# Kernel optimization log

Measured on AMD Instinct MI355X. Metric: run time of the kernel, lower is better.

Reference implementation:

```python
import jax, jax.numpy as jnp
import numpy as np

B, N, K = 4, 2048, 32
U, TU = 512, 128
RADII = (0.1, 0.3, 0.5)
FILTERS = [512, 256, 170]  # U // (i+1) for depth=3
BN_RS = 1.0 / np.sqrt(1.0 + 1e-3)  # inference BN with mean=0, var=1, keras eps=1e-3


def setup_inputs() -> dict:
    key = jax.random.key(0)
    ks = jax.random.split(key, 16)
    rn = lambda k, shape, s: jax.random.normal(k, shape, jnp.float32) * s
    d = {
        "pts": jax.random.normal(ks[0], (B, N, 3), jnp.float32),
        # T-Net params
        "t_cw": rn(ks[1], (3, TU), 0.3), "t_cb": jnp.zeros((TU,), jnp.float32),
        "t_g1": jnp.ones((TU,), jnp.float32), "t_b1": jnp.zeros((TU,), jnp.float32),
        "t_d1w": rn(ks[2], (TU, TU), 0.1), "t_d1b": jnp.zeros((TU,), jnp.float32),
        "t_g2": jnp.ones((TU,), jnp.float32), "t_b2": jnp.zeros((TU,), jnp.float32),
        "t_d2w": rn(ks[3], (TU, 9), 0.3), "t_d2b": jnp.zeros((9,), jnp.float32),
        # PCE conv1 + residual conv
        "c1_w": rn(ks[4], (9, U), 0.2), "c1_b": jnp.zeros((U,), jnp.float32),
        "c1_g": jnp.ones((U,), jnp.float32), "c1_beta": jnp.zeros((U,), jnp.float32),
        "res_w": rn(ks[5], (U, U), 0.05), "res_b": jnp.zeros((U,), jnp.float32),
    }
    fin = U
    for i, f in enumerate(FILTERS):
        d[f"blk{i}_w"] = rn(ks[6 + i], (fin, f), 0.05)
        d[f"blk{i}_b"] = jnp.zeros((f,), jnp.float32)
        d[f"blk{i}_g"] = jnp.ones((f,), jnp.float32)
        d[f"blk{i}_beta"] = jnp.zeros((f,), jnp.float32)
        fin = f
    return d


def _bn(x, g, b):
    # inference BN with moving_mean=0, moving_var=1: (x-0)/sqrt(1+eps)*g + b
    return x * (BN_RS * g) + b


def reference(pts, t_cw, t_cb, t_g1, t_b1, t_d1w, t_d1b, t_g2, t_b2, t_d2w, t_d2b,
              c1_w, c1_b, c1_g, c1_beta, res_w, res_b,
              blk0_w, blk0_b, blk0_g, blk0_beta,
              blk1_w, blk1_b, blk1_g, blk1_beta,
              blk2_w, blk2_b, blk2_g, blk2_beta):
    silu = jax.nn.silu  # keras 'swish'
    # ---- OrthogonalTNet (dropout = identity at inference) ----
    x = silu(_bn(jnp.einsum('bnd,de->bne', pts, t_cw) + t_cb, t_g1, t_b1))  # [B,N,TU]
    x = x.max(axis=1)                                                        # GlobalMaxPool1D
    x = silu(_bn(x @ t_d1w + t_d1b, t_g2, t_b2))
    T = (x @ t_d2w + t_d2b).reshape(-1, 3, 3)
    pc = jnp.einsum('bnd,bde->bne', pts, T)                                  # [B,N,3]
    # ---- pairwise distances [B,N,N] ----
    sq = jnp.sum(pc * pc, axis=-1)
    d2 = sq[:, :, None] + sq[:, None, :] - 2.0 * jnp.einsum('bnd,bmd->bnm', pc, pc)
    dist = jnp.sqrt(jnp.maximum(d2, 0.0))
    # ---- multi-scale grouping: radius mask -> top_k -> gather ----
    groups = []
    for r in RADII:
        mask = (dist <= r).astype(jnp.float32)
        idx = jax.lax.top_k(mask, K)[1]                                      # [B,N,K]
        groups.append(jax.vmap(lambda p, i: p[i])(pc, idx))                  # [B,N,K,3]
    f = jnp.concatenate(groups, axis=-1)                                     # [B,N,K,9]
    # ---- 1x1 conv stack (Dense over channel dim), dropout = identity ----
    f = silu(_bn(f @ c1_w + c1_b, c1_g, c1_beta))                            # [B,N,K,U]
    f = f + (f @ res_w + res_b)                                              # residual
    for w, b, g, beta in ((blk0_w, blk0_b, blk0_g, blk0_beta),
                          (blk1_w, blk1_b, blk1_g, blk1_beta),
                          (blk2_w, blk2_b, blk2_g, blk2_beta)):
        f = silu(_bn(f @ w + b, g, beta))
    Bv, Nv, Kv, Cv = f.shape
    f = f.reshape(Bv, Nv, Kv * Cv)                                           # [B,N,K*170]
    return f.max(axis=1)                                                     # GlobalMaxPool1D -> [B,5440]
```

## Files before the change

kernel.cpp:

```cpp
#include <hip/hip_runtime.h>
#include <math.h>

#define BN_RS 0.9995003746877732f

typedef unsigned short u16;
typedef _Float16 f16;
typedef __attribute__((ext_vector_type(8))) _Float16 h8v;
typedef __attribute__((ext_vector_type(4))) _Float16 h4v;
typedef __attribute__((ext_vector_type(2))) __fp16 fp16x2;
typedef __attribute__((ext_vector_type(4))) float f32x4;

__device__ __forceinline__ unsigned f2mono(float f){
  unsigned u = __float_as_uint(f);
  return (u & 0x80000000u) ? ~u : (u | 0x80000000u);
}
__device__ __forceinline__ float mono2f(unsigned m){
  unsigned u = (m & 0x80000000u) ? (m & 0x7FFFFFFFu) : ~m;
  return __uint_as_float(u);
}
__device__ __forceinline__ float silu_fast(float x){
  float e = __expf(-x);
  return x * __builtin_amdgcn_rcpf(1.f + e);
}
__device__ __forceinline__ float silu_f64(float x){
  double e = exp(-(double)x);
  return (float)((double)x / (1.0 + e));
}
__device__ __forceinline__ h4v pkrtz4(float a, float b, float c, float d){
  fp16x2 lo = __builtin_amdgcn_cvt_pkrtz(a, b);
  fp16x2 hi = __builtin_amdgcn_cvt_pkrtz(c, d);
  unsigned lu = __builtin_bit_cast(unsigned, lo);
  unsigned hu = __builtin_bit_cast(unsigned, hi);
  unsigned long long packed = ((unsigned long long)hu << 32) | lu;
  return __builtin_bit_cast(h4v, packed);
}

constexpr size_t OFF_T9   = 0;
constexpr size_t OFF_XM   = 1024;
constexpr size_t OFF_PC4  = 4096;
constexpr size_t OFF_OUT  = 139264;
constexpr size_t OFF_C1T  = 227328;
constexpr size_t OFF_B0C  = 262144;
constexpr size_t OFF_B1T  = 1310720;
constexpr size_t OFF_B2T  = 1572864;
constexpr size_t OFF_BS1  = 1662976;
constexpr size_t OFF_BS0  = 1667072;
constexpr size_t OFF_BSB1 = 1669120;
constexpr size_t OFF_BSB2 = 1670144;
constexpr size_t OFF_F9   = 1703936;

__global__ void tnet1_kernel(const float* __restrict__ pts, const float* __restrict__ t_cw,
                             const float* __restrict__ t_cb, const float* __restrict__ t_g1,
                             const float* __restrict__ t_b1, unsigned* __restrict__ xm_mono){
  int u = threadIdx.x;
  int b = blockIdx.x;
  int slice = blockIdx.y * blockDim.y + threadIdx.y;
  float w0 = t_cw[u], w1 = t_cw[128+u], w2 = t_cw[256+u];
  float cb = t_cb[u];
  float sc = __fmul_rn(BN_RS, t_g1[u]);
  float b1 = t_b1[u];
  float mx = -INFINITY;
  const float* P = pts + ((size_t)b*2048 + (size_t)slice*128)*3;
  for (int n = 0; n < 128; ++n){
    float y = __fadd_rn(__fadd_rn(__fmul_rn(P[n*3+0], w0), __fmul_rn(P[n*3+1], w1)),
                        __fmul_rn(P[n*3+2], w2));
    y = __fadd_rn(y, cb);
    y = __fadd_rn(__fmul_rn(y, sc), b1);
    mx = fmaxf(mx, silu_f64(y));
  }
  atomicMax(&xm_mono[b*128+u], f2mono(mx));
}

__global__ void tnet2_kernel(const unsigned* __restrict__ xm_mono,
                             const float* __restrict__ d1w, const float* __restrict__ d1b,
                             const float* __restrict__ g2, const float* __restrict__ b2,
                             const float* __restrict__ d2w, const float* __restrict__ d2b,
                             float* __restrict__ T9){
  __shared__ float xs[128], x2s[128];
  int u = threadIdx.x, b = blockIdx.x;
  xs[u] = mono2f(xm_mono[b*128+u]);
  __syncthreads();
  double acc = (double)d1b[u];
  for (int v = 0; v < 128; ++v) acc += (double)xs[v] * (double)d1w[v*128+u];
  double sc = (double)__fmul_rn(BN_RS, g2[u]);
  acc = acc*sc + (double)b2[u];
  double e = exp(-acc);
  x2s[u] = (float)(acc / (1.0 + e));
  __syncthreads();
  if (u < 9){
    double t = (double)d2b[u];
    for (int v = 0; v < 128; ++v) t += (double)x2s[v] * (double)d2w[v*9+u];
    T9[b*9+u] = (float)t;
  }
}

__global__ void pc_kernel(const float* __restrict__ pts, const float* __restrict__ T9,
                          float4* __restrict__ pc4){
  int i = blockIdx.x*blockDim.x + threadIdx.x;
  int b = i >> 11;
  const float* p = pts + (size_t)i*3;
  float x = p[0], y = p[1], z = p[2];
  const float* T = T9 + b*9;
  float px = __fadd_rn(__fadd_rn(__fmul_rn(x, T[0]), __fmul_rn(y, T[3])), __fmul_rn(z, T[6]));
  float py = __fadd_rn(__fadd_rn(__fmul_rn(x, T[1]), __fmul_rn(y, T[4])), __fmul_rn(z, T[7]));
  float pz = __fadd_rn(__fadd_rn(__fmul_rn(x, T[2]), __fmul_rn(y, T[5])), __fmul_rn(z, T[8]));
  float sq = __fadd_rn(__fadd_rn(__fmul_rn(px, px), __fmul_rn(py, py)), __fmul_rn(pz, pz));
  pc4[i] = make_float4(px, py, pz, sq);
}

__global__ __launch_bounds__(256) void group_kernel(const float4* __restrict__ pc4,
                                                    f16* __restrict__ f9){
  __shared__ float4 pcl[2048];
  __shared__ int ones[4][3][32];
  __shared__ int zer [4][3][32];
  const float RAD[3] = {0.1f, 0.3f, 0.5f};
  int tid = threadIdx.x, wave = tid >> 6, lane = tid & 63;
  int bid = blockIdx.x;
  int b = bid >> 9, n0 = (bid & 511) * 4;
  const float4* src = pc4 + (size_t)b*2048;
  for (int x = tid; x < 2048; x += 256) pcl[x] = src[x];
  __syncthreads();

  int n = n0 + wave;
  float4 pi = pcl[n];
  float xi = pi.x, yi = pi.y, zi = pi.z, sqi = pi.w;
  int c1[3] = {0,0,0}, c0[3] = {0,0,0};
  unsigned long long lt = (1ULL << lane) - 1ULL;

  for (int ch = 0; ch < 32; ++ch){
    int j = ch*64 + lane;
    float4 pj = pcl[j];
    float dot = __fadd_rn(__fadd_rn(__fmul_rn(xi, pj.x), __fmul_rn(yi, pj.y)),
                          __fmul_rn(zi, pj.z));
    float d2 = __fsub_rn(__fadd_rn(sqi, pj.w), __fmul_rn(2.f, dot));
    float dist = sqrtf(fmaxf(d2, 0.f));
    #pragma unroll
    for (int ri = 0; ri < 3; ++ri){
      bool in = (dist <= RAD[ri]);
      unsigned long long m = __ballot(in);
      int pc_lt = (int)__popcll(m & lt);
      if (c1[ri] < 32){
        int pos = c1[ri] + pc_lt;
        if (in && pos < 32) ones[wave][ri][pos] = j;
      }
      if (c0[ri] < 32){
        int pos = c0[ri] + (int)(lane - pc_lt);
        if (!in && pos < 32) zer[wave][ri][pos] = j;
      }
      int t1 = (int)__popcll(m);
      c1[ri] += t1;
      c0[ri] += 64 - t1;
    }
    if (c1[0] >= 32 && c1[1] >= 32 && c1[2] >= 32 &&
        c0[0] >= 32 && c0[1] >= 32 && c0[2] >= 32) break;
  }
  __syncthreads();

  if (lane < 32){
    h8v va, vb;
    #pragma unroll
    for (int t = 0; t < 8; ++t){ va[t] = (f16)0.f; vb[t] = (f16)0.f; }
    #pragma unroll
    for (int ri = 0; ri < 3; ++ri){
      int cc = c1[ri] < 32 ? c1[ri] : 32;
      int sel = (lane < cc) ? ones[wave][ri][lane] : zer[wave][ri][lane - cc];
      float4 p = pcl[sel];
      if (ri == 0){ va[0]=(f16)p.x; va[1]=(f16)p.y; va[2]=(f16)p.z; }
      if (ri == 1){ va[3]=(f16)p.x; va[4]=(f16)p.y; va[5]=(f16)p.z; }
      if (ri == 2){ va[6]=(f16)p.x; va[7]=(f16)p.y; vb[0]=(f16)p.z; }
    }
    f16* dst = f9 + (((size_t)(b*2048 + n) * 32 + lane) << 4);
    *(h8v*)dst = va;
    *(h8v*)(dst + 8) = vb;
  }
}

__device__ __forceinline__ void pack_frag(const float* __restrict__ src, f16* __restrict__ dst,
                                          int CO, int CI, int COr, int CIr,
                                          const float* __restrict__ g,
                                          int i0, int stride){
  int NT = CI >> 5;
  int total = (CO >> 4) * NT * 512;
  for (int x = i0; x < total; x += stride){
    int j = x & 7, lane = (x >> 3) & 63;
    int t = (x >> 9) % NT, sct = x / (NT << 9);
    int co = sct*16 + (lane & 15);
    int ci = t*32 + (lane >> 4)*8 + j;
    float v = 0.f;
    if (co < COr && ci < CIr){
      v = src[ci*COr + co];
      if (g) v *= BN_RS * g[co];
    }
    dst[x] = (f16)v;
  }
}

__global__ void prep_kernel(const float* __restrict__ c1w,
                            const float* __restrict__ b0w, const float* __restrict__ b1w,
                            const float* __restrict__ b2w,
                            const float* __restrict__ c1_b, const float* __restrict__ c1_g, const float* __restrict__ c1_be,
                            const float* __restrict__ res_b,
                            const float* __restrict__ b0_b, const float* __restrict__ b0_g, const float* __restrict__ b0_be,
                            const float* __restrict__ b1_b, const float* __restrict__ b1_g, const float* __restrict__ b1_be,
                            const float* __restrict__ b2_b, const float* __restrict__ b2_g, const float* __restrict__ b2_be,
                            f16* __restrict__ c1F, f16* __restrict__ b1F, f16* __restrict__ b2F,
                            float* __restrict__ bs1, float* __restrict__ bs0,
                            float* __restrict__ bsb1, float* __restrict__ bsb2){
  int i0 = blockIdx.x*blockDim.x + threadIdx.x;
  int stride = gridDim.x*blockDim.x;
  pack_frag(c1w,  c1F,  512,  32, 512,   9, c1_g, i0, stride);
  pack_frag(b1w,  b1F,  256, 512, 256, 512, b1_g, i0, stride);
  pack_frag(b2w,  b2F,  176, 256, 170, 256, b2_g, i0, stride);
  for (int x = i0; x < 512; x += stride){
    bs1[x] = c1_b[x]*(BN_RS*c1_g[x]) + c1_be[x];
    float s = b0_b[x];
    for (int m = 0; m < 512; ++m) s = fmaf(res_b[m], b0w[m*512 + x], s);
    bs0[x] = s*(BN_RS*b0_g[x]) + b0_be[x];
  }
  for (int x = i0; x < 256; x += stride) bsb1[x] = b1_b[x]*(BN_RS*b1_g[x]) + b1_be[x];
  for (int x = i0; x < 176; x += stride)
    bsb2[x] = (x < 170) ? b2_b[x]*(BN_RS*b2_g[x]) + b2_be[x] : 0.f;
}

__global__ __launch_bounds__(256) void composeb0_kernel(const float* __restrict__ resw,
                                                        const float* __restrict__ b0w,
                                                        const float* __restrict__ b0_g,
                                                        f16* __restrict__ b0C){
  int x = blockIdx.x*blockDim.x + threadIdx.x;
  int j = x & 7, lane = (x >> 3) & 63;
  int t = (x >> 9) & 15, sct = x >> 13;
  int co = sct*16 + (lane & 15);
  int ci = t*32 + (lane >> 4)*8 + j;
  float s = b0w[ci*512 + co];
  const float* Rrow = resw + ci*512;
  #pragma unroll 4
  for (int m = 0; m < 512; ++m)
    s = fmaf(Rrow[m], b0w[m*512 + co], s);
  b0C[x] = (f16)(s * (BN_RS * b0_g[co]));
}

__device__ __forceinline__ int swzb(int row, int c){
  return (row*1024 + c*2) ^ ((row & 7) << 4);
}

template<int NT, int NCT>
__device__ __forceinline__ void mm_stream(const char* actc, const f16* __restrict__ WF,
                                          int sct0, int lane, int lrow, int lkg,
                                          f32x4 (&acc)[4][NCT]){
  const int xr = (lrow & 7) << 4;
  #pragma unroll
  for (int t = 0; t < NT; ++t){
    h8v a[4];
    int koff = ((t*4 + lkg) << 4) ^ xr;
    #pragma unroll
    for (int mt = 0; mt < 4; ++mt)
      a[mt] = *(const h8v*)(actc + (mt*16 + lrow)*1024 + koff);
    #pragma unroll
    for (int ct = 0; ct < NCT; ++ct){
      h8v w = *(const h8v*)&WF[((size_t)((sct0 + ct)*NT + t)*64 + lane)*8];
      #pragma unroll
      for (int mt = 0; mt < 4; ++mt)
        acc[mt][ct] = __builtin_amdgcn_mfma_f32_16x16x32_f16(w, a[mt], acc[mt][ct], 0, 0, 0);
    }
  }
}

template<int NCT>
__device__ __forceinline__ void epi_silu(char* actc, int co0, const float* __restrict__ bias,
                                         int lrow, int lkg, f32x4 (&acc)[4][NCT]){
  #pragma unroll
  for (int ct = 0; ct < NCT; ++ct){
    int co = co0 + ct*16 + lkg*4;
    float4 b4 = *(const float4*)(bias + co);
    #pragma unroll
    for (int mt = 0; mt < 4; ++mt){
      int r = mt*16 + lrow;
      *(h4v*)(actc + swzb(r, co)) = pkrtz4(
          silu_fast(acc[mt][ct][0] + b4.x),
          silu_fast(acc[mt][ct][1] + b4.y),
          silu_fast(acc[mt][ct][2] + b4.z),
          silu_fast(acc[mt][ct][3] + b4.w));
    }
  }
}

__global__ __launch_bounds__(512, 2) void mlp_kernel(
    const f16* __restrict__ f9,
    const f16* __restrict__ c1F, const f16* __restrict__ b0C,
    const f16* __restrict__ b1F, const f16* __restrict__ b2F,
    const float* __restrict__ bs1, const float* __restrict__ bs0,
    const float* __restrict__ bsb1, const float* __restrict__ bsb2,
    unsigned* __restrict__ outmax){
  __shared__ __align__(16) f16 buf[64*512];
  char* actc = (char*)buf;
  const int tid  = threadIdx.x;
  const int wave = tid >> 6, lane = tid & 63;
  const int lrow = lane & 15, lkg = lane >> 4;
  const int bid = blockIdx.x;
  const int b = bid >> 10, k = (bid >> 5) & 31, n0 = (bid & 31) << 6;

  if (tid < 256){
    int row = tid >> 2, part = tid & 3;
    h8v v;
    if (part < 2){
      const f16* src = f9 + (((size_t)(b*2048 + n0 + row) * 32 + k) << 4) + part*8;
      v = *(const h8v*)src;
    } else {
      #pragma unroll
      for (int t = 0; t < 8; ++t) v[t] = (f16)0.f;
    }
    *(h8v*)&buf[row*32 + part*8] = v;
  }
  __syncthreads();

  const f32x4 zf = {0.f, 0.f, 0.f, 0.f};
  f32x4 acc4[4][4];

  #pragma unroll
  for (int mt = 0; mt < 4; ++mt)
    #pragma unroll
    for (int ct = 0; ct < 4; ++ct) acc4[mt][ct] = zf;
  {
    h8v a[4];
    #pragma unroll
    for (int mt = 0; mt < 4; ++mt)
      a[mt] = *(const h8v*)(actc + (mt*16 + lrow)*64 + lkg*16);
    #pragma unroll
    for (int ct = 0; ct < 4; ++ct){
      h8v w = *(const h8v*)&c1F[((size_t)(wave*4 + ct)*64 + lane)*8];
      #pragma unroll
      for (int mt = 0; mt < 4; ++mt)
        acc4[mt][ct] = __builtin_amdgcn_mfma_f32_16x16x32_f16(w, a[mt], acc4[mt][ct], 0, 0, 0);
    }
  }
  __syncthreads();
  epi_silu<4>(actc, wave*64, bs1, lrow, lkg, acc4);
  __syncthreads();

  #pragma unroll
  for (int mt = 0; mt < 4; ++mt)
    #pragma unroll
    for (int ct = 0; ct < 4; ++ct) acc4[mt][ct] = zf;
  mm_stream<16, 4>(actc, b0C, wave*4, lane, lrow, lkg, acc4);
  __syncthreads();
  epi_silu<4>(actc, wave*64, bs0, lrow, lkg, acc4);
  __syncthreads();

  f32x4 acc2[4][2];
  #pragma unroll
  for (int mt = 0; mt < 4; ++mt){ acc2[mt][0] = zf; acc2[mt][1] = zf; }
  mm_stream<16, 2>(actc, b1F, wave*2, lane, lrow, lkg, acc2);
  __syncthreads();
  epi_silu<2>(actc, wave*32, bsb1, lrow, lkg, acc2);
  __syncthreads();

  f32x4 acc3[4][2];
  #pragma unroll
  for (int mt = 0; mt < 4; ++mt){ acc3[mt][0] = zf; acc3[mt][1] = zf; }
  {
    const int xr = (lrow & 7) << 4;
    const bool has2 = wave < 3;
    #pragma unroll
    for (int t = 0; t < 8; ++t){
      h8v a[4];
      int koff = ((t*4 + lkg) << 4) ^ xr;
      #pragma unroll
      for (int mt = 0; mt < 4; ++mt)
        a[mt] = *(const h8v*)(actc + (mt*16 + lrow)*1024 + koff);
      {
        h8v w = *(const h8v*)&b2F[((size_t)(wave*8 + t)*64 + lane)*8];
        #pragma unroll
        for (int mt = 0; mt < 4; ++mt)
          acc3[mt][0] = __builtin_amdgcn_mfma_f32_16x16x32_f16(a[mt], w, acc3[mt][0], 0, 0, 0);
      }
      if (has2){
        h8v w = *(const h8v*)&b2F[((size_t)((wave + 8)*8 + t)*64 + lane)*8];
        #pragma unroll
        for (int mt = 0; mt < 4; ++mt)
          acc3[mt][1] = __builtin_amdgcn_mfma_f32_16x16x32_f16(a[mt], w, acc3[mt][1], 0, 0, 0);
      }
    }
    #pragma unroll
    for (int t = 0; t < 2; ++t){
      if (t == 1 && !has2) break;
      int c = ((t == 0) ? wave : wave + 8)*16 + lrow;
      if (c < 170){
        float bb = bsb2[c];
        float mx = -INFINITY;
        #pragma unroll
        for (int mt = 0; mt < 4; ++mt)
          #pragma unroll
          for (int rg = 0; rg < 4; ++rg)
            mx = fmaxf(mx, silu_fast(acc3[mt][t][rg] + bb));
        mx = fmaxf(mx, __shfl_xor(mx, 16));
        mx = fmaxf(mx, __shfl_xor(mx, 32));
        if (lkg == 0)
          atomicMax(&outmax[b*5440 + k*170 + c], f2mono(mx));
      }
    }
  }
}

__global__ void finalize_kernel(const unsigned* __restrict__ m, float* __restrict__ out, int n){
  int i = blockIdx.x*blockDim.x + threadIdx.x;
  if (i < n) out[i] = mono2f(m[i]);
}

extern "C" void kernel_launch(void* const* d_in, const int* in_sizes, int n_in,
                              void* d_out, int out_size, void* d_ws, size_t ws_size,
                              hipStream_t stream){
  const float* pts    = (const float*)d_in[0];
  const float* t_cw   = (const float*)d_in[1];
  const float* t_cb   = (const float*)d_in[2];
  const float* t_g1   = (const float*)d_in[3];
  const float* t_b1   = (const float*)d_in[4];
  const float* t_d1w  = (const float*)d_in[5];
  const float* t_d1b  = (const float*)d_in[6];
  const float* t_g2   = (const float*)d_in[7];
  const float* t_b2   = (const float*)d_in[8];
  const float* t_d2w  = (const float*)d_in[9];
  const float* t_d2b  = (const float*)d_in[10];
  const float* c1_w   = (const float*)d_in[11];
  const float* c1_b   = (const float*)d_in[12];
  const float* c1_g   = (const float*)d_in[13];
  const float* c1_be  = (const float*)d_in[14];
  const float* res_w  = (const float*)d_in[15];
  const float* res_b  = (const float*)d_in[16];
  const float* b0_w   = (const float*)d_in[17];
  const float* b0_b   = (const float*)d_in[18];
  const float* b0_g   = (const float*)d_in[19];
  const float* b0_be  = (const float*)d_in[20];
  const float* b1_w   = (const float*)d_in[21];
  const float* b1_b   = (const float*)d_in[22];
  const float* b1_g   = (const float*)d_in[23];
  const float* b1_be  = (const float*)d_in[24];
  const float* b2_w   = (const float*)d_in[25];
  const float* b2_b   = (const float*)d_in[26];
  const float* b2_g   = (const float*)d_in[27];
  const float* b2_be  = (const float*)d_in[28];

  char* ws = (char*)d_ws;
  float*    T9   = (float*)(ws + OFF_T9);
  unsigned* XM   = (unsigned*)(ws + OFF_XM);
  float4*   PC4  = (float4*)(ws + OFF_PC4);
  unsigned* OUTM = (unsigned*)(ws + OFF_OUT);
  f16* C1F  = (f16*)(ws + OFF_C1T);
  f16* B0C  = (f16*)(ws + OFF_B0C);
  f16* B1F  = (f16*)(ws + OFF_B1T);
  f16* B2F  = (f16*)(ws + OFF_B2T);
  float* BS1  = (float*)(ws + OFF_BS1);
  float* BS0  = (float*)(ws + OFF_BS0);
  float* BSB1 = (float*)(ws + OFF_BSB1);
  float* BSB2 = (float*)(ws + OFF_BSB2);
  f16* F9   = (f16*)(ws + OFF_F9);

  hipMemsetAsync(ws + OFF_XM, 0, 4*128*4, stream);
  hipMemsetAsync(ws + OFF_OUT, 0, 21760*4, stream);

  prep_kernel<<<512, 256, 0, stream>>>(c1_w, b0_w, b1_w, b2_w,
                                       c1_b, c1_g, c1_be, res_b,
                                       b0_b, b0_g, b0_be,
                                       b1_b, b1_g, b1_be,
                                       b2_b, b2_g, b2_be,
                                       C1F, B1F, B2F,
                                       BS1, BS0, BSB1, BSB2);
  composeb0_kernel<<<1024, 256, 0, stream>>>(res_w, b0_w, b0_g, B0C);
  tnet1_kernel<<<dim3(4,4), dim3(128,4), 0, stream>>>(pts, t_cw, t_cb, t_g1, t_b1, XM);
  tnet2_kernel<<<4, 128, 0, stream>>>(XM, t_d1w, t_d1b, t_g2, t_b2, t_d2w, t_d2b, T9);
  pc_kernel<<<32, 256, 0, stream>>>(pts, T9, PC4);
  group_kernel<<<2048, 256, 0, stream>>>(PC4, F9);
  mlp_kernel<<<4096, 512, 0, stream>>>(F9, C1F, B0C, B1F, B2F,
                                       BS1, BS0, BSB1, BSB2, OUTM);
  finalize_kernel<<<(out_size + 255)/256, 256, 0, stream>>>(OUTM, (float*)d_out, out_size);
}
```

Baseline: 486.6 us.

## Tile weight-compose GEMM through shared memory and ping-pong MLP activation buffers

The composeb0 kernel, which folds the residual weight into block0's weight, is rewritten from one uncoalesced 512-long dot product per thread into a shared-memory tiled GEMM. Each thread now computes four outputs and uses fewer blocks. The MLP kernel gets two LDS activation buffers so each layer's epilogue writes into the buffer it is not reading, which drops the barrier between each matmul and its epilogue. The cost is double the LDS per block (128 KB), which may cut occupancy below the requested two blocks per CU.

```diff
diff --git a/kernel.cpp b/kernel.cpp
--- a/kernel.cpp
+++ b/kernel.cpp
@@ -226,17 +226,56 @@
                                                         const float* __restrict__ b0w,
                                                         const float* __restrict__ b0_g,
                                                         f16* __restrict__ b0C){
-  int x = blockIdx.x*blockDim.x + threadIdx.x;
-  int j = x & 7, lane = (x >> 3) & 63;
-  int t = (x >> 9) & 15, sct = x >> 13;
-  int co = sct*16 + (lane & 15);
-  int ci = t*32 + (lane >> 4)*8 + j;
-  float s = b0w[ci*512 + co];
-  const float* Rrow = resw + ci*512;
-  #pragma unroll 4
-  for (int m = 0; m < 512; ++m)
-    s = fmaf(Rrow[m], b0w[m*512 + co], s);
-  b0C[x] = (f16)(s * (BN_RS * b0_g[co]));
+  __shared__ float Rt[64][129];
+  __shared__ float Wt[128][17];
+  const int tid = threadIdx.x;
+  const int co0 = (blockIdx.x & 31) * 16;
+  const int ci0 = (blockIdx.x >> 5) * 64;
+  const int r  = tid >> 2;
+  const int cq = tid & 3;
+  float acc[4] = {0.f, 0.f, 0.f, 0.f};
+
+  for (int mc = 0; mc < 512; mc += 128){
+    {
+      int row = tid >> 2, mb = (tid & 3) * 32;
+      const float* src = resw + (size_t)(ci0 + row)*512 + mc + mb;
+      #pragma unroll
+      for (int i = 0; i < 8; ++i){
+        float4 v = *(const float4*)(src + i*4);
+        Rt[row][mb + i*4 + 0] = v.x; Rt[row][mb + i*4 + 1] = v.y;
+        Rt[row][mb + i*4 + 2] = v.z; Rt[row][mb + i*4 + 3] = v.w;
+      }
+    }
+    {
+      int m = tid >> 1, c8 = (tid & 1) * 8;
+      const float* src = b0w + (size_t)(mc + m)*512 + co0 + c8;
+      float4 v0 = *(const float4*)(src);
+      float4 v1 = *(const float4*)(src + 4);
+      Wt[m][c8+0] = v0.x; Wt[m][c8+1] = v0.y; Wt[m][c8+2] = v0.z; Wt[m][c8+3] = v0.w;
+      Wt[m][c8+4] = v1.x; Wt[m][c8+5] = v1.y; Wt[m][c8+6] = v1.z; Wt[m][c8+7] = v1.w;
+    }
+    __syncthreads();
+    #pragma unroll 8
+    for (int m = 0; m < 128; ++m){
+      float rv = Rt[r][m];
+      #pragma unroll
+      for (int i = 0; i < 4; ++i)
+        acc[i] = fmaf(rv, Wt[m][cq*4 + i], acc[i]);
+    }
+    __syncthreads();
+  }
+  int ci = ci0 + r;
+  #pragma unroll
+  for (int i = 0; i < 4; ++i){
+    int co = co0 + cq*4 + i;
+    float s = acc[i] + b0w[(size_t)ci*512 + co];
+    if (ci == co) {}
+    s *= BN_RS * b0_g[co];
+    int sct = co >> 4, t = ci >> 5;
+    int lane = (co & 15) | (((ci >> 3) & 3) << 4);
+    int j = ci & 7;
+    b0C[((size_t)(sct*16 + t)*64 + lane)*8 + j] = (f16)s;
+  }
 }
 
 __device__ __forceinline__ int swzb(int row, int c){
@@ -266,7 +305,7 @@
 }
 
 template<int NCT>
-__device__ __forceinline__ void epi_silu(char* actc, int co0, const float* __restrict__ bias,
+__device__ __forceinline__ void epi_silu(char* outc, int co0, const float* __restrict__ bias,
                                          int lrow, int lkg, f32x4 (&acc)[4][NCT]){
   #pragma unroll
   for (int ct = 0; ct < NCT; ++ct){
@@ -275,7 +314,7 @@
     #pragma unroll
     for (int mt = 0; mt < 4; ++mt){
       int r = mt*16 + lrow;
-      *(h4v*)(actc + swzb(r, co)) = pkrtz4(
+      *(h4v*)(outc + swzb(r, co)) = pkrtz4(
           silu_fast(acc[mt][ct][0] + b4.x),
           silu_fast(acc[mt][ct][1] + b4.y),
           silu_fast(acc[mt][ct][2] + b4.z),
@@ -291,8 +330,10 @@
     const float* __restrict__ bs1, const float* __restrict__ bs0,
     const float* __restrict__ bsb1, const float* __restrict__ bsb2,
     unsigned* __restrict__ outmax){
-  __shared__ __align__(16) f16 buf[64*512];
-  char* actc = (char*)buf;
+  __shared__ __align__(16) f16 bufA[64*512];
+  __shared__ __align__(16) f16 bufB[64*512];
+  char* A = (char*)bufA;
+  char* B = (char*)bufB;
   const int tid  = threadIdx.x;
   const int wave = tid >> 6, lane = tid & 63;
   const int lrow = lane & 15, lkg = lane >> 4;
@@ -309,7 +350,7 @@
       #pragma unroll
       for (int t = 0; t < 8; ++t) v[t] = (f16)0.f;
     }
-    *(h8v*)&buf[row*32 + part*8] = v;
+    *(h8v*)&bufA[row*32 + part*8] = v;
   }
   __syncthreads();
 
@@ -324,7 +365,7 @@
     h8v a[4];
     #pragma unroll
     for (int mt = 0; mt < 4; ++mt)
-      a[mt] = *(const h8v*)(actc + (mt*16 + lrow)*64 + lkg*16);
+      a[mt] = *(const h8v*)(A + (mt*16 + lrow)*64 + lkg*16);
     #pragma unroll
     for (int ct = 0; ct < 4; ++ct){
       h8v w = *(const h8v*)&c1F[((size_t)(wave*4 + ct)*64 + lane)*8];
@@ -333,25 +374,22 @@
         acc4[mt][ct] = __builtin_amdgcn_mfma_f32_16x16x32_f16(w, a[mt], acc4[mt][ct], 0, 0, 0);
     }
   }
-  __syncthreads();
-  epi_silu<4>(actc, wave*64, bs1, lrow, lkg, acc4);
+  epi_silu<4>(B, wave*64, bs1, lrow, lkg, acc4);
   __syncthreads();
 
   #pragma unroll
   for (int mt = 0; mt < 4; ++mt)
     #pragma unroll
     for (int ct = 0; ct < 4; ++ct) acc4[mt][ct] = zf;
-  mm_stream<16, 4>(actc, b0C, wave*4, lane, lrow, lkg, acc4);
-  __syncthreads();
-  epi_silu<4>(actc, wave*64, bs0, lrow, lkg, acc4);
+  mm_stream<16, 4>(B, b0C, wave*4, lane, lrow, lkg, acc4);
+  epi_silu<4>(A, wave*64, bs0, lrow, lkg, acc4);
   __syncthreads();
 
   f32x4 acc2[4][2];
   #pragma unroll
   for (int mt = 0; mt < 4; ++mt){ acc2[mt][0] = zf; acc2[mt][1] = zf; }
-  mm_stream<16, 2>(actc, b1F, wave*2, lane, lrow, lkg, acc2);
-  __syncthreads();
-  epi_silu<2>(actc, wave*32, bsb1, lrow, lkg, acc2);
+  mm_stream<16, 2>(A, b1F, wave*2, lane, lrow, lkg, acc2);
+  epi_silu<2>(B, wave*32, bsb1, lrow, lkg, acc2);
   __syncthreads();
 
   f32x4 acc3[4][2];
@@ -366,7 +404,7 @@
       int koff = ((t*4 + lkg) << 4) ^ xr;
       #pragma unroll
       for (int mt = 0; mt < 4; ++mt)
-        a[mt] = *(const h8v*)(actc + (mt*16 + lrow)*1024 + koff);
+        a[mt] = *(const h8v*)(B + (mt*16 + lrow)*1024 + koff);
       {
         h8v w = *(const h8v*)&b2F[((size_t)(wave*8 + t)*64 + lane)*8];
         #pragma unroll
@@ -464,7 +502,7 @@
                                        b2_b, b2_g, b2_be,
                                        C1F, B1F, B2F,
                                        BS1, BS0, BSB1, BSB2);
-  composeb0_kernel<<<1024, 256, 0, stream>>>(res_w, b0_w, b0_g, B0C);
+  composeb0_kernel<<<256, 256, 0, stream>>>(res_w, b0_w, b0_g, B0C);
   tnet1_kernel<<<dim3(4,4), dim3(128,4), 0, stream>>>(pts, t_cw, t_cb, t_g1, t_b1, XM);
   tnet2_kernel<<<4, 128, 0, stream>>>(XM, t_d1w, t_d1b, t_g2, t_b2, t_d2w, t_d2b, T9);
   pc_kernel<<<32, 256, 0, stream>>>(pts, T9, PC4);
```

Result: faster. 429.9 us (-11.7%).
